# Optimization experiments

Measured on AMD Instinct MI355X. Metric: run time of the kernel, lower is better.

Reference implementation:

```python
import jax, jax.numpy as jnp
import numpy as np

N_QUBITS = 6
N_LAYERS = 2
QSVT_DEGREE = 3
DT_RANK = max(N_QUBITS // 2, 1)
OUT_DIM = 3 * N_QUBITS
PI = np.float32(np.pi)
DT_MIN, DT_MAX = 1e-3, 0.1
BATCH, SEQ = 256, 512


def _ry_mat(theta):
    c = jnp.cos(theta / 2)
    s = jnp.sin(theta / 2)
    row0 = jnp.stack([c, -s], axis=-1)
    row1 = jnp.stack([s, c], axis=-1)
    return jnp.stack([row0, row1], axis=-2).astype(jnp.complex64)


def _rz_mat(theta):
    e = jnp.exp(-0.5j * theta.astype(jnp.complex64))
    z = jnp.zeros_like(e)
    row0 = jnp.stack([e, z], axis=-1)
    row1 = jnp.stack([z, jnp.conj(e)], axis=-1)
    return jnp.stack([row0, row1], axis=-2)


def _rx_mat(theta):
    c = jnp.cos(theta / 2).astype(jnp.complex64)
    s = jnp.sin(theta / 2).astype(jnp.complex64)
    row0 = jnp.stack([c, -1j * s], axis=-1)
    row1 = jnp.stack([-1j * s, c], axis=-1)
    return jnp.stack([row0, row1], axis=-2)


def _apply1(state, mat, w):
    # state: (B, 2, ..., 2) tensor over N_QUBITS axes; mat: (2,2) or batched (B,2,2)
    state = jnp.moveaxis(state, 1 + w, -1)
    if mat.ndim == 3:
        state = jnp.einsum('bij,b...j->b...i', mat, state)
    else:
        state = jnp.einsum('ij,b...j->b...i', mat, state)
    return jnp.moveaxis(state, -1, 1 + w)


def _cnot(state, c, t):
    state = jnp.moveaxis(state, (1 + c, 1 + t), (-2, -1))
    state = state.at[..., 1, :].set(state[..., 1, ::-1])
    return jnp.moveaxis(state, (-2, -1), (1 + c, 1 + t))


def _crx(state, theta, c, t):
    state = jnp.moveaxis(state, (1 + c, 1 + t), (-2, -1))
    m = _rx_mat(theta)
    state = state.at[..., 1, :].set(jnp.einsum('ij,...j->...i', m, state[..., 1, :]))
    return jnp.moveaxis(state, (-2, -1), (1 + c, 1 + t))


def _circuit(h, x, dt, circuit_params, poly_coeffs, qsvt_params):
    """Batched statevector simulation of the selective QSVT + unified ansatz qnode."""
    n = N_QUBITS
    B = h.shape[0]
    state = jnp.zeros((B,) + (2,) * n, jnp.complex64)
    state = state.at[(slice(None),) + (0,) * n].set(1.0 + 0.0j)
    # 1) state encoding RY(h[t-1])
    for i in range(n):
        state = _apply1(state, _ry_mat(h[:, i]), i)
    # 2) Delta-modulated QSVT: RZ rotations + bidirectional CNOT ring per degree
    qidx = 0
    n_qp = n * QSVT_DEGREE
    for deg in range(QSVT_DEGREE + 1):
        coeff = poly_coeffs[deg]
        for i in range(n):
            if qidx < n_qp:
                ang = coeff * dt[:, i] * qsvt_params[qidx] * PI
                qidx += 1
            else:
                ang = coeff * dt[:, i] * PI
            state = _apply1(state, _rz_mat(ang), i)
        for i in range(n - 1):
            state = _cnot(state, i, i + 1)
        state = _cnot(state, n - 1, 0)
        for i in range(n - 1, 0, -1):
            state = _cnot(state, i, i - 1)
    # 3) unified variational ansatz
    p = 0
    for _ in range(N_LAYERS):
        for i in range(n):
            state = _apply1(state, _rx_mat(circuit_params[p]), i)
            state = _apply1(state, _ry_mat(circuit_params[p + 1]), i)
            state = _apply1(state, _rz_mat(circuit_params[p + 2]), i)
            p += 3
        for i in range(n):
            state = _crx(state, circuit_params[p], i, (i + 1) % n)
            p += 1
        for i in range(n - 1, -1, -1):
            state = _crx(state, circuit_params[p], i, (i - 1) % n)
            p += 1
    # 4) Delta-modulated input RY(x * dt)
    for i in range(n):
        state = _apply1(state, _ry_mat(x[:, i] * dt[:, i]), i)
    # 5) Pauli X/Y/Z expectation values per qubit
    xs, ys, zs = [], [], []
    for i in range(n):
        s = jnp.moveaxis(state, 1 + i, 1).reshape(B, 2, -1)
        z = jnp.sum(jnp.conj(s[:, 0]) * s[:, 1], axis=-1)
        xs.append(2.0 * jnp.real(z))
        ys.append(2.0 * jnp.imag(z))
        zs.append(jnp.sum(jnp.abs(s[:, 0]) ** 2 - jnp.abs(s[:, 1]) ** 2, axis=-1))
    return jnp.stack(xs + ys + zs, axis=-1).astype(jnp.float32)  # (B, 3n)


def setup_inputs() -> dict:
    key = jax.random.key(0)
    ks = jax.random.split(key, 8)
    angles = jax.random.uniform(ks[0], (BATCH, SEQ, N_QUBITS), jnp.float32) * PI
    Wx = jax.random.normal(ks[1], (DT_RANK + 2 * N_QUBITS, N_QUBITS), jnp.float32) / np.float32(np.sqrt(N_QUBITS))
    Wdt = jax.random.normal(ks[2], (N_QUBITS, DT_RANK), jnp.float32) / np.float32(np.sqrt(DT_RANK))
    dt = jnp.exp(jax.random.uniform(ks[3], (N_QUBITS,), jnp.float32) * np.float32(np.log(DT_MAX) - np.log(DT_MIN)) + np.float32(np.log(DT_MIN)))
    bdt = dt + jnp.log(-jnp.expm1(-dt))
    poly_coeffs = jax.random.normal(ks[4], (QSVT_DEGREE + 1,), jnp.float32) * 0.1
    qsvt_params = jax.random.normal(ks[5], (N_QUBITS * QSVT_DEGREE,), jnp.float32) * 0.1
    circuit_params = jax.random.normal(ks[6], (5 * N_QUBITS * N_LAYERS,), jnp.float32) * 0.1
    D = jnp.ones((OUT_DIM,), jnp.float32)
    Wc = jax.random.normal(ks[7], (OUT_DIM, N_QUBITS), jnp.float32) / np.float32(np.sqrt(N_QUBITS))
    return {"angles": angles, "Wx": Wx, "Wdt": Wdt, "bdt": bdt, "poly_coeffs": poly_coeffs, "qsvt_params": qsvt_params, "circuit_params": circuit_params, "D": D, "Wc": Wc}


def reference(angles, Wx, Wdt, bdt, poly_coeffs, qsvt_params, circuit_params, D, Wc):
    x_dbc = angles @ Wx.T  # (B,S, dt_rank + 2n)
    dt_raw = x_dbc[..., :DT_RANK]
    # B slice computed in the original but never used in forward
    C = x_dbc[..., DT_RANK + N_QUBITS:]
    dt_angles = jnp.tanh(jax.nn.softplus(dt_raw @ Wdt.T + bdt)) * PI  # (B,S,n)
    # quantum part is detached in the original (detach().cpu() before the qnode)
    sg = jax.lax.stop_gradient
    xs = (jnp.moveaxis(sg(angles), 1, 0), jnp.moveaxis(sg(dt_angles), 1, 0))
    cp, pc, qp = sg(circuit_params), sg(poly_coeffs), sg(qsvt_params)
    h0 = jnp.zeros((angles.shape[0], N_QUBITS), jnp.float32)

    def step(h, xt):
        x_t, dt_t = xt
        meas = _circuit(h, x_t, dt_t, cp, pc, qp)
        return meas[:, 2 * N_QUBITS:], meas  # carry = PauliZ block

    _, meas = jax.lax.scan(step, h0, xs)
    h_full = jnp.moveaxis(meas, 0, 1)  # (B,S,3n)
    return (C @ Wc.T) * h_full + D * jnp.concatenate([angles] * 3, axis=-1)
```

## Files before the change

kernel.cpp:

```cpp
#include <hip/hip_runtime.h>
#include <math.h>

#define BATCH 256
#define SEQ 512
#define SDS 54
#define PI_F 3.14159265358979323846f
#define INV2PI_F 0.15915494309189535f

template<int CTRL>
__device__ __forceinline__ float fdpp(float v) {
    return __int_as_float(__builtin_amdgcn_mov_dpp(__float_as_int(v), CTRL, 0xF, 0xF, true));
}
template<int L>
__device__ __forceinline__ float rdl(float v) {
    return __int_as_float(__builtin_amdgcn_readlane(__float_as_int(v), L));
}
__device__ __forceinline__ float rdlv(float v, int l) {
    return __int_as_float(__builtin_amdgcn_readlane(__float_as_int(v), l));
}
__device__ __forceinline__ float x1f(float v) { return fdpp<0xB1>(v); }
__device__ __forceinline__ float x2f(float v) { return fdpp<0x4E>(v); }
__device__ __forceinline__ float x4f(float v) { return fdpp<0x141>(fdpp<0x1B>(v)); }
__device__ __forceinline__ float x8f(float v) { return fdpp<0x128>(v); }
#if __has_builtin(__builtin_amdgcn_permlane16_swap)
__device__ __forceinline__ float sum16(float v) {
    typedef unsigned int u2v __attribute__((ext_vector_type(2)));
    u2v r = __builtin_amdgcn_permlane16_swap(__float_as_uint(v), __float_as_uint(v), false, false);
    return __uint_as_float(r[0]) + __uint_as_float(r[1]);
}
#else
__device__ __forceinline__ float sum16(float v) {
    return v + __int_as_float(__builtin_amdgcn_ds_swizzle(__float_as_int(v), (16 << 10) | 0x1F));
}
#endif
#if __has_builtin(__builtin_amdgcn_permlane32_swap)
__device__ __forceinline__ float sum32(float v) {
    typedef unsigned int u2v __attribute__((ext_vector_type(2)));
    u2v r = __builtin_amdgcn_permlane32_swap(__float_as_uint(v), __float_as_uint(v), false, false);
    return __uint_as_float(r[0]) + __uint_as_float(r[1]);
}
#else
__device__ __forceinline__ float sum32(float v) { return v + __shfl_xor(v, 32, 64); }
#endif
__device__ __forceinline__ float redsum64(float v) {
    v += fdpp<0x128>(v);
    v += fdpp<0x124>(v);
    v += fdpp<0x122>(v);
    v += fdpp<0x121>(v);
    v = sum16(v);
    v = sum32(v);
    return v;
}
__device__ __forceinline__ float xorf(float v, int m) {
    return __int_as_float(__float_as_int(v) ^ m);
}
__device__ __forceinline__ void wg_barrier_lds() {
    __builtin_amdgcn_sched_barrier(0);
    __builtin_amdgcn_s_waitcnt(0xC07F);
    __builtin_amdgcn_s_barrier();
    __builtin_amdgcn_sched_barrier(0);
}
__device__ __forceinline__ int permf(int x) {
    const int cs[11] = {0,1,2,3,4,5,5,4,3,2,1};
    const int ts[11] = {1,2,3,4,5,0,4,3,2,1,0};
#pragma unroll
    for (int k = 10; k >= 0; k--) {
        int cb = (x >> (5 - cs[k])) & 1;
        x ^= cb << (5 - ts[k]);
    }
    return x;
}
__device__ __forceinline__ void cmul4(const float* c,
    float vr, float vi, float ar, float ai, float br, float bi, float cr, float ci,
    float& nr, float& ni) {
    nr = c[0]*vr - c[1]*vi + c[2]*ar - c[3]*ai + c[4]*br - c[5]*bi + c[6]*cr - c[7]*ci;
    ni = c[0]*vi + c[1]*vr + c[2]*ai + c[3]*ar + c[4]*bi + c[5]*br + c[6]*ci + c[7]*cr;
}
__device__ __forceinline__ void ringapply(const float* rc,
    float vr, float vi, float br, float bi, float cr, float ci, float dr, float di,
    float& nr, float& ni) {
    nr = rc[0]*vr - rc[1]*bi - rc[2]*ci + rc[3]*dr;
    ni = rc[0]*vi + rc[1]*br + rc[2]*cr + rc[3]*di;
}

__global__ __launch_bounds__(256) void prep_kernel(
    const float* __restrict__ angles, const float* __restrict__ Wx,
    const float* __restrict__ Wdt, const float* __restrict__ bdt,
    const float* __restrict__ D, const float* __restrict__ Wc,
    float* __restrict__ sd)
{
    int gid = blockIdx.x * blockDim.x + threadIdx.x;
    if (gid >= BATCH * SEQ) return;
    const float* a = angles + (size_t)gid * 6;
    float ang[6];
#pragma unroll
    for (int i = 0; i < 6; i++) ang[i] = a[i];
    float dtr[3];
#pragma unroll
    for (int r = 0; r < 3; r++) {
        float s = 0.f;
#pragma unroll
        for (int k = 0; k < 6; k++) s += ang[k] * Wx[r * 6 + k];
        dtr[r] = s;
    }
    float* rec = sd + (size_t)gid * SDS;
    float dtv[6];
#pragma unroll
    for (int i = 0; i < 6; i++) {
        float x = bdt[i];
#pragma unroll
        for (int r = 0; r < 3; r++) x += dtr[r] * Wdt[i * 3 + r];
        float sp = (x > 15.f) ? x : log1pf(expf(x));
        dtv[i] = tanhf(sp) * PI_F;
        rec[i] = dtv[i];
        float th = ang[i] * dtv[i];
        rec[6 + i]  = 0.5f * cosf(th);
        rec[12 + i] = 0.5f * sinf(th);
    }
    float C[6];
#pragma unroll
    for (int i = 0; i < 6; i++) {
        float s = 0.f;
#pragma unroll
        for (int k = 0; k < 6; k++) s += ang[k] * Wx[(9 + i) * 6 + k];
        C[i] = s;
    }
#pragma unroll
    for (int j = 0; j < 18; j++) {
        float s = 0.f;
#pragma unroll
        for (int i = 0; i < 6; i++) s += C[i] * Wc[j * 6 + i];
        rec[18 + j] = (j < 6 || j >= 12) ? 2.f * s : s;
        rec[36 + j] = D[j] * ang[j % 6];
    }
}

__global__ __launch_bounds__(64) void umat_kernel(const float* __restrict__ cp,
                                                  float2* __restrict__ um)
{
    const int lane = threadIdx.x;
    const int col = blockIdx.x;
    int bitv[6];
#pragma unroll
    for (int i = 0; i < 6; i++) bitv[i] = (lane >> (5 - i)) & 1;

    float qc[2][3][8], rc[2][6][4];
#pragma unroll
    for (int l = 0; l < 2; l++) {
        float g00r[6], g00i[6], g01r[6], g01i[6], g10r[6], g10i[6], g11r[6], g11i[6];
#pragma unroll
        for (int i = 0; i < 6; i++) {
            float ax = cp[l * 30 + i * 3 + 0];
            float ay = cp[l * 30 + i * 3 + 1];
            float az = cp[l * 30 + i * 3 + 2];
            float ca = cosf(0.5f * ax), sa = sinf(0.5f * ax);
            float cb = cosf(0.5f * ay), sb = sinf(0.5f * ay);
            float cg = cosf(0.5f * az), sg = sinf(0.5f * az);
            float m00r = cb * ca, m00i =  sb * sa;
            float m01r = -sb * ca, m01i = -cb * sa;
            float m10r =  sb * ca, m10i = -cb * sa;
            float m11r =  cb * ca, m11i = -sb * sa;
            g00r[i] = cg * m00r + sg * m00i; g00i[i] = cg * m00i - sg * m00r;
            g01r[i] = cg * m01r + sg * m01i; g01i[i] = cg * m01i - sg * m01r;
            g10r[i] = cg * m10r - sg * m10i; g10i[i] = cg * m10i + sg * m10r;
            g11r[i] = cg * m11r - sg * m11i; g11i[i] = cg * m11i + sg * m11r;
        }
#pragma unroll
        for (int pp = 0; pp < 3; pp++) {
            int aq = 2 * pp, bq = 2 * pp + 1;
            float dar = bitv[aq] ? g11r[aq] : g00r[aq], dai = bitv[aq] ? g11i[aq] : g00i[aq];
            float oar = bitv[aq] ? g10r[aq] : g01r[aq], oai = bitv[aq] ? g10i[aq] : g01i[aq];
            float dbr = bitv[bq] ? g11r[bq] : g00r[bq], dbi = bitv[bq] ? g11i[bq] : g00i[bq];
            float obr = bitv[bq] ? g10r[bq] : g01r[bq], obi = bitv[bq] ? g10i[bq] : g01i[bq];
            qc[l][pp][0] = dar * dbr - dai * dbi;  qc[l][pp][1] = dar * dbi + dai * dbr;
            qc[l][pp][2] = oar * dbr - oai * dbi;  qc[l][pp][3] = oar * dbi + oai * dbr;
            qc[l][pp][4] = dar * obr - dai * obi;  qc[l][pp][5] = dar * obi + dai * obr;
            qc[l][pp][6] = oar * obr - oai * obi;  qc[l][pp][7] = oar * obi + oai * obr;
        }
        const int Aq[6] = {0, 2, 4, 5, 3, 1};
        const int Bq[6] = {1, 3, 5, 4, 2, 0};
#pragma unroll
        for (int o = 0; o < 6; o++) {
            float tha = (o < 3) ? cp[l * 30 + 18 + 2 * o]     : cp[l * 30 + 24 + 2 * (o - 3)];
            float thb = (o < 3) ? cp[l * 30 + 18 + 2 * o + 1] : cp[l * 30 + 24 + 2 * (o - 3) + 1];
            float ca = cosf(0.5f * tha), sa = sinf(0.5f * tha);
            float cb = cosf(0.5f * thb), sb = sinf(0.5f * thb);
            int ba = bitv[Aq[o]], bb = bitv[Bq[o]];
            float mx0 = ba ? ca : 1.f, sae = ba ? sa : 0.f;
            float ny0 = bb ? cb : 1.f, sbe = bb ? sb : 0.f;
            rc[l][o][0] = ny0 * mx0; rc[l][o][1] = -ny0 * sae;
            rc[l][o][2] = -mx0 * sbe; rc[l][o][3] = -sae * sbe;
        }
    }

    float re = (lane == col) ? 1.f : 0.f;
    float im = 0.f;
    auto p1q = [&](int mi, int mj, const float* c) {
        float ar = __shfl_xor(re, mi, 64), ai = __shfl_xor(im, mi, 64);
        float br = __shfl_xor(re, mj, 64), bi = __shfl_xor(im, mj, 64);
        float cr = __shfl_xor(re, mi | mj, 64), ci = __shfl_xor(im, mi | mj, 64);
        float nr, ni;
        cmul4(c, re, im, ar, ai, br, bi, cr, ci, nr, ni);
        re = nr; im = ni;
    };
    auto rng = [&](int mb, int mc, const float* c) {
        float br = __shfl_xor(re, mb, 64), bi = __shfl_xor(im, mb, 64);
        float cr = __shfl_xor(re, mc, 64), ci = __shfl_xor(im, mc, 64);
        float dr = __shfl_xor(re, mb | mc, 64), di = __shfl_xor(im, mb | mc, 64);
        float nr, ni;
        ringapply(c, re, im, br, bi, cr, ci, dr, di, nr, ni);
        re = nr; im = ni;
    };
#pragma unroll
    for (int l = 0; l < 2; l++) {
        p1q(32, 16, qc[l][0]);
        p1q(8, 4, qc[l][1]);
        p1q(2, 1, qc[l][2]);
        rng(16, 8, rc[l][0]);
        rng(4, 2, rc[l][1]);
        rng(1, 32, rc[l][2]);
        rng(2, 4, rc[l][3]);
        rng(8, 16, rc[l][4]);
        rng(32, 1, rc[l][5]);
    }
    um[(size_t)lane * 64 + col] = make_float2(re, im);
}

#define CMACR(AR, AI, UU, SR, SI)            \
    AR = fmaf((UU).x, (SR), AR);             \
    AR = fmaf(-(UU).y, (SI), AR);            \
    AI = fmaf((UU).x, (SI), AI);             \
    AI = fmaf((UU).y, (SR), AI);

__global__ __launch_bounds__(256, 1) void step_kernel(
    const float* __restrict__ sd, const float* __restrict__ pcf,
    const float* __restrict__ qp, const float2* __restrict__ um,
    float* __restrict__ out)
{
    __shared__ float2 sPart[2][4][64];
    const int tid = threadIdx.x;
    const int wave = tid >> 6;
    const int lane = tid & 63;
    const int b = blockIdx.x;

    int bitv[6];
#pragma unroll
    for (int i = 0; i < 6; i++) bitv[i] = (lane >> (5 - i)) & 1;
    int sflip[6];
    float sgnf[6];
#pragma unroll
    for (int q = 0; q < 6; q++) {
        sflip[q] = bitv[q] ? (int)0x80000000 : 0;
        sgnf[q]  = bitv[q] ? -1.f : 1.f;
    }
    const float w0 = bitv[0] ? -2.f : 0.f;
    const float w1 = bitv[1] ? -2.f : 0.f;

    const int jbase = wave * 16;
    float2 row[16];
#pragma unroll
    for (int jj = 0; jj < 16; jj++) row[jj] = um[(size_t)lane * 64 + jbase + jj];

    float A[6], sel[6];
    {
        int x1 = permf(lane), x2 = permf(x1), x3 = permf(x2), x4 = permf(x3);
#pragma unroll
        for (int i = 0; i < 6; i++) {
            float u0 = pcf[0] * PI_F * qp[0 * 6 + i];
            float u1 = pcf[1] * PI_F * qp[1 * 6 + i];
            float u2 = pcf[2] * PI_F * qp[2 * 6 + i];
            float u3 = pcf[3] * PI_F;
            float t1 = ((x1 >> (5 - i)) & 1) ? 0.5f : -0.5f;
            float t2 = ((x2 >> (5 - i)) & 1) ? 0.5f : -0.5f;
            float t3 = ((x3 >> (5 - i)) & 1) ? 0.5f : -0.5f;
            float t4 = ((x4 >> (5 - i)) & 1) ? 0.5f : -0.5f;
            A[i] = u3 * t1 + u2 * t2 + u1 * t3 + u0 * t4;
            sel[i] = (float)((x4 >> (5 - i)) & 1);
        }
    }

    auto b6 = [&](float v) -> float {
        float g;
        g = x1f(v); v = fmaf(sgnf[5], v, g);
        g = x2f(v); v = fmaf(sgnf[4], v, g);
        g = x4f(v); v = fmaf(sgnf[3], v, g);
        g = x8f(v); v = fmaf(sgnf[2], v, g);
        v = fmaf(w1, v, sum16(v));
        v = fmaf(w0, v, sum32(v));
        return v;
    };

    const float* sdb = sd + (size_t)b * SEQ * SDS;
    float* outb = out + (size_t)b * SEQ * 18;

    float hh0 = 0.f, hh1 = 0.f, hh2 = 0.f, hh3 = 0.f, hh4 = 0.f, hh5 = 0.f;

    float buf0[18], buf1[18], buf2[18];
    auto ldrec = [&](float (&dst)[18], int t) {
        const float2* p2 = (const float2*)(sdb + (size_t)t * SDS);
#pragma unroll
        for (int k = 0; k < 9; k++) {
            float2 v = p2[k];
            dst[2 * k] = v.x; dst[2 * k + 1] = v.y;
        }
    };
    ldrec(buf0, 0);
    ldrec(buf1, 1);

    float sphC, cphC;
    {
        float phi = A[0]*buf0[0] + A[1]*buf0[1] + A[2]*buf0[2]
                  + A[3]*buf0[3] + A[4]*buf0[4] + A[5]*buf0[5];
        float u = phi * INV2PI_F;
        u = u - floorf(u);
        sphC = __builtin_amdgcn_sinf(u);
        cphC = __builtin_amdgcn_cosf(u);
    }

    auto body = [&](float (&cur)[18], float (&nxt)[18], float (&far)[18], int t) {
        const int pp = t & 1;
        ldrec(far, (t + 2 < SEQ) ? t + 2 : SEQ - 1);

        float ss0 = __builtin_amdgcn_sinf(hh0 * INV2PI_F), cc0 = __builtin_amdgcn_cosf(hh0 * INV2PI_F);
        float ss1 = __builtin_amdgcn_sinf(hh1 * INV2PI_F), cc1 = __builtin_amdgcn_cosf(hh1 * INV2PI_F);
        float ss2 = __builtin_amdgcn_sinf(hh2 * INV2PI_F), cc2 = __builtin_amdgcn_cosf(hh2 * INV2PI_F);
        float ss3 = __builtin_amdgcn_sinf(hh3 * INV2PI_F), cc3 = __builtin_amdgcn_cosf(hh3 * INV2PI_F);
        float ss4 = __builtin_amdgcn_sinf(hh4 * INV2PI_F), cc4 = __builtin_amdgcn_cosf(hh4 * INV2PI_F);
        float ss5 = __builtin_amdgcn_sinf(hh5 * INV2PI_F), cc5 = __builtin_amdgcn_cosf(hh5 * INV2PI_F);
        float f0 = fmaf(sel[0], ss0 - cc0, cc0);
        float f1 = fmaf(sel[1], ss1 - cc1, cc1);
        float f2 = fmaf(sel[2], ss2 - cc2, cc2);
        float f3 = fmaf(sel[3], ss3 - cc3, cc3);
        float f4 = fmaf(sel[4], ss4 - cc4, cc4);
        float f5 = fmaf(sel[5], ss5 - cc5, cc5);
        float prod = ((f0 * f1) * (f2 * f3)) * (f4 * f5);
        float pr = prod * cphC, pi = prod * sphC;

        {
            float phi = A[0]*nxt[0] + A[1]*nxt[1] + A[2]*nxt[2]
                      + A[3]*nxt[3] + A[4]*nxt[4] + A[5]*nxt[5];
            float u = phi * INV2PI_F;
            u = u - floorf(u);
            sphC = __builtin_amdgcn_sinf(u);
            cphC = __builtin_amdgcn_cosf(u);
        }

        float ar0 = 0.f, ai0 = 0.f, ar1 = 0.f, ai1 = 0.f;
#pragma unroll
        for (int jj = 0; jj < 16; jj += 2) {
            float sr0 = rdlv(pr, jbase + jj);
            float si0 = rdlv(pi, jbase + jj);
            float sr1 = rdlv(pr, jbase + jj + 1);
            float si1 = rdlv(pi, jbase + jj + 1);
            CMACR(ar0, ai0, row[jj], sr0, si0)
            CMACR(ar1, ai1, row[jj + 1], sr1, si1)
        }
        sPart[pp][wave][lane] = make_float2(ar0 + ar1, ai0 + ai1);
        wg_barrier_lds();
        float2 q0v = sPart[pp][0][lane], q1v = sPart[pp][1][lane];
        float2 q2v = sPart[pp][2][lane], q3v = sPart[pp][3][lane];
        float re = (q0v.x + q1v.x) + (q2v.x + q3v.x);
        float im = (q0v.y + q1v.y) + (q2v.y + q3v.y);

        float P  = fmaf(re, re, im * im);
        float Wp = b6(P);
        float Z0 = rdl<32>(Wp), Z1 = rdl<16>(Wp), Z2 = rdl<8>(Wp);
        float Z3 = rdl<4>(Wp),  Z4 = rdl<2>(Wp),  Z5 = rdl<1>(Wp);

        float g32r = sum32(re) - re, g32i = sum32(im) - im;
        float g16r = sum16(re) - re, g16i = sum16(im) - im;
        float g8r  = x8f(re),        g8i  = x8f(im);
        float g4r  = x4f(re),        g4i  = x4f(im);
        float g2r  = x2f(re),        g2i  = x2f(im);
        float g1r  = x1f(re),        g1i  = x1f(im);

        float X0 = redsum64(fmaf(re, g32r, im * g32i));
        float X1 = redsum64(fmaf(re, g16r, im * g16i));
        float X2 = redsum64(fmaf(re, g8r,  im * g8i));
        float X3 = redsum64(fmaf(re, g4r,  im * g4i));
        float X4 = redsum64(fmaf(re, g2r,  im * g2i));
        float X5 = redsum64(fmaf(re, g1r,  im * g1i));

        hh0 = cur[6]  * Z0 - cur[12] * X0;
        hh1 = cur[7]  * Z1 - cur[13] * X1;
        hh2 = cur[8]  * Z2 - cur[14] * X2;
        hh3 = cur[9]  * Z3 - cur[15] * X3;
        hh4 = cur[10] * Z4 - cur[16] * X4;
        hh5 = cur[11] * Z5 - cur[17] * X5;

        float* o = outb + (size_t)t * 18;
        if (wave == 0) {
            if (lane == 0) {
                float2* o2 = (float2*)o;
                o2[0] = make_float2(Z0, Z1); o2[1] = make_float2(Z2, Z3);
                o2[2] = make_float2(Z4, Z5); o2[3] = make_float2(X0, X1);
                o2[4] = make_float2(X2, X3); o2[5] = make_float2(X4, X5);
            }
        } else if (wave == 1) {
            float Y0 = redsum64(xorf(fmaf(re, g32i, -(im * g32r)), sflip[0]));
            float Y1 = redsum64(xorf(fmaf(re, g16i, -(im * g16r)), sflip[1]));
            if (lane == 0) ((float2*)(o + 12))[0] = make_float2(Y0, Y1);
        } else if (wave == 2) {
            float Y2 = redsum64(xorf(fmaf(re, g8i, -(im * g8r)), sflip[2]));
            float Y3 = redsum64(xorf(fmaf(re, g4i, -(im * g4r)), sflip[3]));
            if (lane == 0) ((float2*)(o + 14))[0] = make_float2(Y2, Y3);
        } else {
            float Y4 = redsum64(xorf(fmaf(re, g2i, -(im * g2r)), sflip[4]));
            float Y5 = redsum64(xorf(fmaf(re, g1i, -(im * g1r)), sflip[5]));
            if (lane == 0) ((float2*)(o + 16))[0] = make_float2(Y4, Y5);
        }
    };

    for (int t = 0; t < 510; t += 3) {
        body(buf0, buf1, buf2, t);
        body(buf1, buf2, buf0, t + 1);
        body(buf2, buf0, buf1, t + 2);
    }
    body(buf0, buf1, buf2, 510);
    body(buf1, buf2, buf0, 511);
}
#undef CMACR

__global__ __launch_bounds__(256) void post_kernel(
    const float* __restrict__ sd, float* __restrict__ out)
{
    int gid = blockIdx.x * blockDim.x + threadIdx.x;
    if (gid >= BATCH * SEQ) return;
    const float* rec = sd + (size_t)gid * SDS;
    float* o = out + (size_t)gid * 18;

    float zxy[18];
    {
        const float2* o2 = (const float2*)o;
#pragma unroll
        for (int k = 0; k < 9; k++) {
            float2 v = o2[k];
            zxy[2 * k] = v.x; zxy[2 * k + 1] = v.y;
        }
    }
    float r[54];
    {
        const float2* r2 = (const float2*)rec;
#pragma unroll
        for (int k = 3; k < 27; k++) {
            float2 v = r2[k];
            r[2 * k] = v.x; r[2 * k + 1] = v.y;
        }
    }
    float res[18];
#pragma unroll
    for (int q = 0; q < 6; q++) {
        float Z = zxy[q], X = zxy[6 + q], Y = zxy[12 + q];
        float c = r[6 + q], s = r[12 + q];
        float px = c * X + s * Z;
        float hq = c * Z - s * X;
        res[q]      = fmaf(r[18 + q], px, r[36 + q]);
        res[6 + q]  = fmaf(r[24 + q], Y,  r[42 + q]);
        res[12 + q] = fmaf(r[30 + q], hq, r[48 + q]);
    }
    float2* ow = (float2*)o;
#pragma unroll
    for (int k = 0; k < 9; k++) ow[k] = make_float2(res[2 * k], res[2 * k + 1]);
}

extern "C" void kernel_launch(void* const* d_in, const int* in_sizes, int n_in,
                              void* d_out, int out_size, void* d_ws, size_t ws_size,
                              hipStream_t stream) {
    const float* angles = (const float*)d_in[0];
    const float* Wx     = (const float*)d_in[1];
    const float* Wdt    = (const float*)d_in[2];
    const float* bdt    = (const float*)d_in[3];
    const float* pc     = (const float*)d_in[4];
    const float* qp     = (const float*)d_in[5];
    const float* cp     = (const float*)d_in[6];
    const float* D      = (const float*)d_in[7];
    const float* Wc     = (const float*)d_in[8];
    float* sd  = (float*)d_ws;
    float2* um = (float2*)(sd + (size_t)BATCH * SEQ * SDS);
    float* out = (float*)d_out;

    umat_kernel<<<64, 64, 0, stream>>>(cp, um);
    prep_kernel<<<(BATCH * SEQ) / 256, 256, 0, stream>>>(angles, Wx, Wdt, bdt, D, Wc, sd);
    step_kernel<<<BATCH, 256, 0, stream>>>(sd, pc, qp, um, out);
    post_kernel<<<(BATCH * SEQ) / 256, 256, 0, stream>>>(sd, out);
}
```

Before: 708.3 us.

## Apply ansatz gates directly in a single-wave step kernel instead of dense unitary

```diff
diff --git a/kernel.cpp b/kernel.cpp
--- a/kernel.cpp
+++ b/kernel.cpp
@@ -6,6 +6,8 @@
 #define SDS 54
 #define PI_F 3.14159265358979323846f
 #define INV2PI_F 0.15915494309189535f
+#define K_HALF_INV2PI 0.07957747154594767f
+#define FOURPI_F 12.566370614359172f
 
 template<int CTRL>
 __device__ __forceinline__ float fdpp(float v) {
@@ -15,13 +17,10 @@
 __device__ __forceinline__ float rdl(float v) {
     return __int_as_float(__builtin_amdgcn_readlane(__float_as_int(v), L));
 }
-__device__ __forceinline__ float rdlv(float v, int l) {
-    return __int_as_float(__builtin_amdgcn_readlane(__float_as_int(v), l));
-}
-__device__ __forceinline__ float x1f(float v) { return fdpp<0xB1>(v); }
-__device__ __forceinline__ float x2f(float v) { return fdpp<0x4E>(v); }
-__device__ __forceinline__ float x4f(float v) { return fdpp<0x141>(fdpp<0x1B>(v)); }
-__device__ __forceinline__ float x8f(float v) { return fdpp<0x128>(v); }
+template<int M>
+__device__ __forceinline__ float swz(float v) {
+    return __int_as_float(__builtin_amdgcn_ds_swizzle(__float_as_int(v), (M << 10) | 0x1F));
+}
 #if __has_builtin(__builtin_amdgcn_permlane16_swap)
 __device__ __forceinline__ float sum16(float v) {
     typedef unsigned int u2v __attribute__((ext_vector_type(2)));
@@ -29,9 +28,7 @@
     return __uint_as_float(r[0]) + __uint_as_float(r[1]);
 }
 #else
-__device__ __forceinline__ float sum16(float v) {
-    return v + __int_as_float(__builtin_amdgcn_ds_swizzle(__float_as_int(v), (16 << 10) | 0x1F));
-}
+__device__ __forceinline__ float sum16(float v) { return v + swz<16>(v); }
 #endif
 #if __has_builtin(__builtin_amdgcn_permlane32_swap)
 __device__ __forceinline__ float sum32(float v) {
@@ -42,6 +39,18 @@
 #else
 __device__ __forceinline__ float sum32(float v) { return v + __shfl_xor(v, 32, 64); }
 #endif
+template<int M>
+__device__ __forceinline__ float exg(float v) {
+    if constexpr (M == 1)       return fdpp<0xB1>(v);
+    else if constexpr (M == 2)  return fdpp<0x4E>(v);
+    else if constexpr (M == 3)  return fdpp<0x1B>(v);
+    else if constexpr (M == 4)  return fdpp<0x141>(fdpp<0x1B>(v));
+    else if constexpr (M == 8)  return fdpp<0x128>(v);
+    else if constexpr (M == 32) return sum32(v) - v;
+    else if constexpr (M == 48) { float w = swz<16>(v); return sum32(w) - w; }
+    else if constexpr (M == 33) { float w = fdpp<0xB1>(v); return sum32(w) - w; }
+    else                        return swz<M>(v);
+}
 __device__ __forceinline__ float redsum64(float v) {
     v += fdpp<0x128>(v);
     v += fdpp<0x124>(v);
@@ -54,12 +63,6 @@
 __device__ __forceinline__ float xorf(float v, int m) {
     return __int_as_float(__float_as_int(v) ^ m);
 }
-__device__ __forceinline__ void wg_barrier_lds() {
-    __builtin_amdgcn_sched_barrier(0);
-    __builtin_amdgcn_s_waitcnt(0xC07F);
-    __builtin_amdgcn_s_barrier();
-    __builtin_amdgcn_sched_barrier(0);
-}
 __device__ __forceinline__ int permf(int x) {
     const int cs[11] = {0,1,2,3,4,5,5,4,3,2,1};
     const int ts[11] = {1,2,3,4,5,0,4,3,2,1,0};
@@ -81,6 +84,24 @@
     float& nr, float& ni) {
     nr = rc[0]*vr - rc[1]*bi - rc[2]*ci + rc[3]*dr;
     ni = rc[0]*vi + rc[1]*br + rc[2]*cr + rc[3]*di;
+}
+template<int MI, int MJ>
+__device__ __forceinline__ void p1qS(float& re, float& im, const float* c) {
+    float ar = exg<MI>(re),      ai = exg<MI>(im);
+    float br = exg<MJ>(re),      bi = exg<MJ>(im);
+    float cr = exg<MI | MJ>(re), ci = exg<MI | MJ>(im);
+    float nr, ni;
+    cmul4(c, re, im, ar, ai, br, bi, cr, ci, nr, ni);
+    re = nr; im = ni;
+}
+template<int MB, int MC>
+__device__ __forceinline__ void rngS(float& re, float& im, const float* c) {
+    float br = exg<MB>(re),      bi = exg<MB>(im);
+    float cr = exg<MC>(re),      ci = exg<MC>(im);
+    float dr = exg<MB | MC>(re), di = exg<MB | MC>(im);
+    float nr, ni;
+    ringapply(c, re, im, br, bi, cr, ci, dr, di, nr, ni);
+    re = nr; im = ni;
 }
 
 __global__ __launch_bounds__(256) void prep_kernel(
@@ -114,8 +135,8 @@
         dtv[i] = tanhf(sp) * PI_F;
         rec[i] = dtv[i];
         float th = ang[i] * dtv[i];
-        rec[6 + i]  = 0.5f * cosf(th);
-        rec[12 + i] = 0.5f * sinf(th);
+        rec[6 + i]  = K_HALF_INV2PI * cosf(th);
+        rec[12 + i] = K_HALF_INV2PI * sinf(th);
     }
     float C[6];
 #pragma unroll
@@ -130,19 +151,31 @@
         float s = 0.f;
 #pragma unroll
         for (int i = 0; i < 6; i++) s += C[i] * Wc[j * 6 + i];
-        rec[18 + j] = (j < 6 || j >= 12) ? 2.f * s : s;
+        rec[18 + j] = (j < 6 || j >= 12) ? FOURPI_F * s : s;
         rec[36 + j] = D[j] * ang[j % 6];
     }
 }
 
-__global__ __launch_bounds__(64) void umat_kernel(const float* __restrict__ cp,
-                                                  float2* __restrict__ um)
+__global__ __launch_bounds__(64, 1) void step_kernel(
+    const float* __restrict__ sd, const float* __restrict__ pcf,
+    const float* __restrict__ qp, const float* __restrict__ cp,
+    float* __restrict__ out)
 {
     const int lane = threadIdx.x;
-    const int col = blockIdx.x;
+    const int b = blockIdx.x;
+
     int bitv[6];
 #pragma unroll
     for (int i = 0; i < 6; i++) bitv[i] = (lane >> (5 - i)) & 1;
+    int sflip[6];
+    float sgnf[6];
+#pragma unroll
+    for (int q = 0; q < 6; q++) {
+        sflip[q] = bitv[q] ? (int)0x80000000 : 0;
+        sgnf[q]  = bitv[q] ? -1.f : 1.f;
+    }
+    const float w0 = bitv[0] ? -2.f : 0.f;
+    const float w1 = bitv[1] ? -2.f : 0.f;
 
     float qc[2][3][8], rc[2][6][4];
 #pragma unroll
@@ -193,74 +226,6 @@
         }
     }
 
-    float re = (lane == col) ? 1.f : 0.f;
-    float im = 0.f;
-    auto p1q = [&](int mi, int mj, const float* c) {
-        float ar = __shfl_xor(re, mi, 64), ai = __shfl_xor(im, mi, 64);
-        float br = __shfl_xor(re, mj, 64), bi = __shfl_xor(im, mj, 64);
-        float cr = __shfl_xor(re, mi | mj, 64), ci = __shfl_xor(im, mi | mj, 64);
-        float nr, ni;
-        cmul4(c, re, im, ar, ai, br, bi, cr, ci, nr, ni);
-        re = nr; im = ni;
-    };
-    auto rng = [&](int mb, int mc, const float* c) {
-        float br = __shfl_xor(re, mb, 64), bi = __shfl_xor(im, mb, 64);
-        float cr = __shfl_xor(re, mc, 64), ci = __shfl_xor(im, mc, 64);
-        float dr = __shfl_xor(re, mb | mc, 64), di = __shfl_xor(im, mb | mc, 64);
-        float nr, ni;
-        ringapply(c, re, im, br, bi, cr, ci, dr, di, nr, ni);
-        re = nr; im = ni;
-    };
-#pragma unroll
-    for (int l = 0; l < 2; l++) {
-        p1q(32, 16, qc[l][0]);
-        p1q(8, 4, qc[l][1]);
-        p1q(2, 1, qc[l][2]);
-        rng(16, 8, rc[l][0]);
-        rng(4, 2, rc[l][1]);
-        rng(1, 32, rc[l][2]);
-        rng(2, 4, rc[l][3]);
-        rng(8, 16, rc[l][4]);
-        rng(32, 1, rc[l][5]);
-    }
-    um[(size_t)lane * 64 + col] = make_float2(re, im);
-}
-
-#define CMACR(AR, AI, UU, SR, SI)            \
-    AR = fmaf((UU).x, (SR), AR);             \
-    AR = fmaf(-(UU).y, (SI), AR);            \
-    AI = fmaf((UU).x, (SI), AI);             \
-    AI = fmaf((UU).y, (SR), AI);
-
-__global__ __launch_bounds__(256, 1) void step_kernel(
-    const float* __restrict__ sd, const float* __restrict__ pcf,
-    const float* __restrict__ qp, const float2* __restrict__ um,
-    float* __restrict__ out)
-{
-    __shared__ float2 sPart[2][4][64];
-    const int tid = threadIdx.x;
-    const int wave = tid >> 6;
-    const int lane = tid & 63;
-    const int b = blockIdx.x;
-
-    int bitv[6];
-#pragma unroll
-    for (int i = 0; i < 6; i++) bitv[i] = (lane >> (5 - i)) & 1;
-    int sflip[6];
-    float sgnf[6];
-#pragma unroll
-    for (int q = 0; q < 6; q++) {
-        sflip[q] = bitv[q] ? (int)0x80000000 : 0;
-        sgnf[q]  = bitv[q] ? -1.f : 1.f;
-    }
-    const float w0 = bitv[0] ? -2.f : 0.f;
-    const float w1 = bitv[1] ? -2.f : 0.f;
-
-    const int jbase = wave * 16;
-    float2 row[16];
-#pragma unroll
-    for (int jj = 0; jj < 16; jj++) row[jj] = um[(size_t)lane * 64 + jbase + jj];
-
     float A[6], sel[6];
     {
         int x1 = permf(lane), x2 = permf(x1), x3 = permf(x2), x4 = permf(x3);
@@ -274,17 +239,17 @@
             float t2 = ((x2 >> (5 - i)) & 1) ? 0.5f : -0.5f;
             float t3 = ((x3 >> (5 - i)) & 1) ? 0.5f : -0.5f;
             float t4 = ((x4 >> (5 - i)) & 1) ? 0.5f : -0.5f;
-            A[i] = u3 * t1 + u2 * t2 + u1 * t3 + u0 * t4;
+            A[i] = (u3 * t1 + u2 * t2 + u1 * t3 + u0 * t4) * INV2PI_F;
             sel[i] = (float)((x4 >> (5 - i)) & 1);
         }
     }
 
     auto b6 = [&](float v) -> float {
         float g;
-        g = x1f(v); v = fmaf(sgnf[5], v, g);
-        g = x2f(v); v = fmaf(sgnf[4], v, g);
-        g = x4f(v); v = fmaf(sgnf[3], v, g);
-        g = x8f(v); v = fmaf(sgnf[2], v, g);
+        g = exg<1>(v); v = fmaf(sgnf[5], v, g);
+        g = exg<2>(v); v = fmaf(sgnf[4], v, g);
+        g = exg<4>(v); v = fmaf(sgnf[3], v, g);
+        g = exg<8>(v); v = fmaf(sgnf[2], v, g);
         v = fmaf(w1, v, sum16(v));
         v = fmaf(w0, v, sum32(v));
         return v;
@@ -309,24 +274,22 @@
 
     float sphC, cphC;
     {
-        float phi = A[0]*buf0[0] + A[1]*buf0[1] + A[2]*buf0[2]
-                  + A[3]*buf0[3] + A[4]*buf0[4] + A[5]*buf0[5];
-        float u = phi * INV2PI_F;
+        float u = A[0]*buf0[0] + A[1]*buf0[1] + A[2]*buf0[2]
+                + A[3]*buf0[3] + A[4]*buf0[4] + A[5]*buf0[5];
         u = u - floorf(u);
         sphC = __builtin_amdgcn_sinf(u);
         cphC = __builtin_amdgcn_cosf(u);
     }
 
     auto body = [&](float (&cur)[18], float (&nxt)[18], float (&far)[18], int t) {
-        const int pp = t & 1;
         ldrec(far, (t + 2 < SEQ) ? t + 2 : SEQ - 1);
 
-        float ss0 = __builtin_amdgcn_sinf(hh0 * INV2PI_F), cc0 = __builtin_amdgcn_cosf(hh0 * INV2PI_F);
-        float ss1 = __builtin_amdgcn_sinf(hh1 * INV2PI_F), cc1 = __builtin_amdgcn_cosf(hh1 * INV2PI_F);
-        float ss2 = __builtin_amdgcn_sinf(hh2 * INV2PI_F), cc2 = __builtin_amdgcn_cosf(hh2 * INV2PI_F);
-        float ss3 = __builtin_amdgcn_sinf(hh3 * INV2PI_F), cc3 = __builtin_amdgcn_cosf(hh3 * INV2PI_F);
-        float ss4 = __builtin_amdgcn_sinf(hh4 * INV2PI_F), cc4 = __builtin_amdgcn_cosf(hh4 * INV2PI_F);
-        float ss5 = __builtin_amdgcn_sinf(hh5 * INV2PI_F), cc5 = __builtin_amdgcn_cosf(hh5 * INV2PI_F);
+        float ss0 = __builtin_amdgcn_sinf(hh0), cc0 = __builtin_amdgcn_cosf(hh0);
+        float ss1 = __builtin_amdgcn_sinf(hh1), cc1 = __builtin_amdgcn_cosf(hh1);
+        float ss2 = __builtin_amdgcn_sinf(hh2), cc2 = __builtin_amdgcn_cosf(hh2);
+        float ss3 = __builtin_amdgcn_sinf(hh3), cc3 = __builtin_amdgcn_cosf(hh3);
+        float ss4 = __builtin_amdgcn_sinf(hh4), cc4 = __builtin_amdgcn_cosf(hh4);
+        float ss5 = __builtin_amdgcn_sinf(hh5), cc5 = __builtin_amdgcn_cosf(hh5);
         float f0 = fmaf(sel[0], ss0 - cc0, cc0);
         float f1 = fmaf(sel[1], ss1 - cc1, cc1);
         float f2 = fmaf(sel[2], ss2 - cc2, cc2);
@@ -334,45 +297,40 @@
         float f4 = fmaf(sel[4], ss4 - cc4, cc4);
         float f5 = fmaf(sel[5], ss5 - cc5, cc5);
         float prod = ((f0 * f1) * (f2 * f3)) * (f4 * f5);
-        float pr = prod * cphC, pi = prod * sphC;
+        float re = prod * cphC, im = prod * sphC;
 
         {
-            float phi = A[0]*nxt[0] + A[1]*nxt[1] + A[2]*nxt[2]
-                      + A[3]*nxt[3] + A[4]*nxt[4] + A[5]*nxt[5];
-            float u = phi * INV2PI_F;
+            float u = A[0]*nxt[0] + A[1]*nxt[1] + A[2]*nxt[2]
+                    + A[3]*nxt[3] + A[4]*nxt[4] + A[5]*nxt[5];
             u = u - floorf(u);
             sphC = __builtin_amdgcn_sinf(u);
             cphC = __builtin_amdgcn_cosf(u);
         }
 
-        float ar0 = 0.f, ai0 = 0.f, ar1 = 0.f, ai1 = 0.f;
-#pragma unroll
-        for (int jj = 0; jj < 16; jj += 2) {
-            float sr0 = rdlv(pr, jbase + jj);
-            float si0 = rdlv(pi, jbase + jj);
-            float sr1 = rdlv(pr, jbase + jj + 1);
-            float si1 = rdlv(pi, jbase + jj + 1);
-            CMACR(ar0, ai0, row[jj], sr0, si0)
-            CMACR(ar1, ai1, row[jj + 1], sr1, si1)
-        }
-        sPart[pp][wave][lane] = make_float2(ar0 + ar1, ai0 + ai1);
-        wg_barrier_lds();
-        float2 q0v = sPart[pp][0][lane], q1v = sPart[pp][1][lane];
-        float2 q2v = sPart[pp][2][lane], q3v = sPart[pp][3][lane];
-        float re = (q0v.x + q1v.x) + (q2v.x + q3v.x);
-        float im = (q0v.y + q1v.y) + (q2v.y + q3v.y);
+#pragma unroll
+        for (int l = 0; l < 2; l++) {
+            p1qS<32, 16>(re, im, qc[l][0]);
+            p1qS<8, 4>(re, im, qc[l][1]);
+            p1qS<2, 1>(re, im, qc[l][2]);
+            rngS<16, 8>(re, im, rc[l][0]);
+            rngS<4, 2>(re, im, rc[l][1]);
+            rngS<1, 32>(re, im, rc[l][2]);
+            rngS<2, 4>(re, im, rc[l][3]);
+            rngS<8, 16>(re, im, rc[l][4]);
+            rngS<32, 1>(re, im, rc[l][5]);
+        }
 
         float P  = fmaf(re, re, im * im);
         float Wp = b6(P);
         float Z0 = rdl<32>(Wp), Z1 = rdl<16>(Wp), Z2 = rdl<8>(Wp);
         float Z3 = rdl<4>(Wp),  Z4 = rdl<2>(Wp),  Z5 = rdl<1>(Wp);
 
-        float g32r = sum32(re) - re, g32i = sum32(im) - im;
-        float g16r = sum16(re) - re, g16i = sum16(im) - im;
-        float g8r  = x8f(re),        g8i  = x8f(im);
-        float g4r  = x4f(re),        g4i  = x4f(im);
-        float g2r  = x2f(re),        g2i  = x2f(im);
-        float g1r  = x1f(re),        g1i  = x1f(im);
+        float g32r = exg<32>(re), g32i = exg<32>(im);
+        float g16r = exg<16>(re), g16i = exg<16>(im);
+        float g8r  = exg<8>(re),  g8i  = exg<8>(im);
+        float g4r  = exg<4>(re),  g4i  = exg<4>(im);
+        float g2r  = exg<2>(re),  g2i  = exg<2>(im);
+        float g1r  = exg<1>(re),  g1i  = exg<1>(im);
 
         float X0 = redsum64(fmaf(re, g32r, im * g32i));
         float X1 = redsum64(fmaf(re, g16r, im * g16i));
@@ -388,26 +346,20 @@
         hh4 = cur[10] * Z4 - cur[16] * X4;
         hh5 = cur[11] * Z5 - cur[17] * X5;
 
-        float* o = outb + (size_t)t * 18;
-        if (wave == 0) {
-            if (lane == 0) {
-                float2* o2 = (float2*)o;
-                o2[0] = make_float2(Z0, Z1); o2[1] = make_float2(Z2, Z3);
-                o2[2] = make_float2(Z4, Z5); o2[3] = make_float2(X0, X1);
-                o2[4] = make_float2(X2, X3); o2[5] = make_float2(X4, X5);
-            }
-        } else if (wave == 1) {
-            float Y0 = redsum64(xorf(fmaf(re, g32i, -(im * g32r)), sflip[0]));
-            float Y1 = redsum64(xorf(fmaf(re, g16i, -(im * g16r)), sflip[1]));
-            if (lane == 0) ((float2*)(o + 12))[0] = make_float2(Y0, Y1);
-        } else if (wave == 2) {
-            float Y2 = redsum64(xorf(fmaf(re, g8i, -(im * g8r)), sflip[2]));
-            float Y3 = redsum64(xorf(fmaf(re, g4i, -(im * g4r)), sflip[3]));
-            if (lane == 0) ((float2*)(o + 14))[0] = make_float2(Y2, Y3);
-        } else {
-            float Y4 = redsum64(xorf(fmaf(re, g2i, -(im * g2r)), sflip[4]));
-            float Y5 = redsum64(xorf(fmaf(re, g1i, -(im * g1r)), sflip[5]));
-            if (lane == 0) ((float2*)(o + 16))[0] = make_float2(Y4, Y5);
+        float Y0 = redsum64(xorf(fmaf(re, g32i, -(im * g32r)), sflip[0]));
+        float Y1 = redsum64(xorf(fmaf(re, g16i, -(im * g16r)), sflip[1]));
+        float Y2 = redsum64(xorf(fmaf(re, g8i,  -(im * g8r)),  sflip[2]));
+        float Y3 = redsum64(xorf(fmaf(re, g4i,  -(im * g4r)),  sflip[3]));
+        float Y4 = redsum64(xorf(fmaf(re, g2i,  -(im * g2r)),  sflip[4]));
+        float Y5 = redsum64(xorf(fmaf(re, g1i,  -(im * g1r)),  sflip[5]));
+
+        if (lane == 0) {
+            float2* o2 = (float2*)(outb + (size_t)t * 18);
+            o2[0] = make_float2(Z0, Z1); o2[1] = make_float2(Z2, Z3);
+            o2[2] = make_float2(Z4, Z5); o2[3] = make_float2(X0, X1);
+            o2[4] = make_float2(X2, X3); o2[5] = make_float2(X4, X5);
+            o2[6] = make_float2(Y0, Y1); o2[7] = make_float2(Y2, Y3);
+            o2[8] = make_float2(Y4, Y5);
         }
     };
 
@@ -419,7 +371,6 @@
     body(buf0, buf1, buf2, 510);
     body(buf1, buf2, buf0, 511);
 }
-#undef CMACR
 
 __global__ __launch_bounds__(256) void post_kernel(
     const float* __restrict__ sd, float* __restrict__ out)
@@ -476,11 +427,9 @@
     const float* D      = (const float*)d_in[7];
     const float* Wc     = (const float*)d_in[8];
     float* sd  = (float*)d_ws;
-    float2* um = (float2*)(sd + (size_t)BATCH * SEQ * SDS);
     float* out = (float*)d_out;
 
-    umat_kernel<<<64, 64, 0, stream>>>(cp, um);
     prep_kernel<<<(BATCH * SEQ) / 256, 256, 0, stream>>>(angles, Wx, Wdt, bdt, D, Wc, sd);
-    step_kernel<<<BATCH, 256, 0, stream>>>(sd, pc, qp, um, out);
+    step_kernel<<<BATCH, 64, 0, stream>>>(sd, pc, qp, cp, out);
     post_kernel<<<(BATCH * SEQ) / 256, 256, 0, stream>>>(sd, out);
 }
```

Result: slower. 1.072 ms (+51.3%).
